# Kernel optimization log

Hardware: AMD Instinct MI355X
Metric: run time of the kernel (lower is better)

Reference implementation:

```python
import jax, jax.numpy as jnp
import numpy as np

MC = 16384
N_STEPS = 120
PERIOD = 30
N_MAT = 4
N_STR = 21
WIDTH_DIFF = 50
WIDTH_VAN = 30
WIDTH_EXO = 20
N_HIDDEN = 3  # n_layers=4 -> input layer + 3 hidden layers + output layer
R = 0.05
TIMEGRID = jnp.asarray(np.linspace(0.0, 1.0, N_STEPS + 1).astype(np.float32))
STRIKES = jnp.asarray(np.linspace(0.8, 1.2, N_STR).astype(np.float32))


def _init_net(key, d_in, width, d_out):
    ks = jax.random.split(key, 6)
    f = lambda k, shape, fan: jax.random.normal(k, shape, jnp.float32) / np.sqrt(fan).astype(np.float32)
    return dict(
        W0=f(ks[0], (N_MAT, d_in, width), d_in),
        b0=f(ks[1], (N_MAT, width), width),
        hW=f(ks[2], (N_MAT, N_HIDDEN, width, width), width),
        hb=f(ks[3], (N_MAT, N_HIDDEN, width), width),
        Wo=f(ks[4], (N_MAT, width, d_out), width),
        bo=f(ks[5], (N_MAT, d_out), width),
    )


def setup_inputs() -> dict:
    key = jax.random.key(0)
    kz, kd, kv, ke = jax.random.split(key, 4)
    inp = {
        "S0": jnp.ones((1,), jnp.float32),
        "z": jax.random.normal(kz, (MC, N_STEPS), jnp.float32),
    }
    for name, net in (("d", _init_net(kd, 2, WIDTH_DIFF, 1)),
                      ("v", _init_net(kv, 2, WIDTH_VAN, N_STR * N_MAT)),
                      ("e", _init_net(ke, N_STEPS + 2, WIDTH_EXO, 1))):
        for pn, arr in net.items():
            inp[name + pn] = arr
    inp["MC_samples"] = MC
    inp["ind_T"] = N_STEPS
    inp["period_length"] = PERIOD
    return inp


def _mlp(x, W0, b0, hW, hb, Wo, bo, softplus_out):
    h = jax.nn.relu(x @ W0 + b0)
    for k in range(hW.shape[0]):  # static small number of hidden layers
        h = jax.nn.relu(h @ hW[k] + hb[k])
    y = h @ Wo + bo
    return jax.nn.softplus(y) if softplus_out else y


def _forward(S0, z, dW0, db0, dhW, dhb, dWo, dbo,
             vW0, vb0, vhW, vhb, vWo, vbo,
             eW0, eb0, ehW, ehb, eWo, ebo,
             MC_samples, ind_T, period_length, remat=False):
    sg = jax.lax.stop_gradient
    S_init = jnp.ones((MC_samples, 1), jnp.float32) * S0
    path0 = jnp.zeros((MC_samples, N_STEPS + 1), jnp.float32).at[:, 0].set(S_init[:, 0])
    zeros_mat = jnp.zeros((N_MAT, N_STR), jnp.float32)

    def step(carry, i):
        S_old, cv_v, cv_e, run_max, path, pv, pvv = carry
        idx = (i - 1) // period_length
        t0 = TIMEGRID[i - 1]
        h = TIMEGRID[i] - TIMEGRID[i - 1]
        sqh = jnp.sqrt(h)
        dWn = sqh * jax.lax.dynamic_slice_in_dim(z, i - 1, 1, 1)  # (MC,1)
        t = jnp.full_like(S_old, t0)
        diff = _mlp(jnp.concatenate([t, S_old], 1),
                    dW0[idx], db0[idx], dhW[idx], dhb[idx], dWo[idx], dbo[idx], True)
        Sd, diffd = sg(S_old), sg(diff)
        S_new = (S_old
                 + R * S_old * h / (1.0 + R * Sd * sqh)
                 + S_old * diff * dWn / (1.0 + Sd * diffd * sqh))
        disc = jnp.exp(-R * t0)
        cv_v = cv_v + disc * Sd * diffd * dWn * _mlp(
            jnp.concatenate([t, Sd], 1),
            vW0[idx], vb0[idx], vhW[idx], vhb[idx], vWo[idx], vbo[idx], False)
        cv_e = cv_e + disc * Sd * diffd * dWn * _mlp(
            jnp.concatenate([t, path], 1),
            eW0[idx], eb0[idx], ehW[idx], ehb[idx], eWo[idx], ebo[idx], False)
        path = jax.lax.dynamic_update_slice(path, sg(S_new), (0, i))
        run_max = jnp.maximum(run_max, S_new)
        # vanilla prices at maturities (i multiple of period_length)
        ind_m = i // period_length - 1
        disc_i = jnp.exp(-R * TIMEGRID[i])
        cv_row = jax.lax.dynamic_slice_in_dim(
            cv_v.reshape(MC_samples, N_MAT, N_STR), ind_m, 1, 1)[:, 0, :]
        pr = disc_i * jnp.maximum(S_new - STRIKES[None, :], 0.0) - cv_row  # (MC, N_STR)
        is_mat = (i % period_length) == 0
        pv = jnp.where(is_mat, jax.lax.dynamic_update_index_in_dim(pv, pr.mean(0), ind_m, 0), pv)
        pvv = jnp.where(is_mat, jax.lax.dynamic_update_index_in_dim(pvv, jnp.var(pr, axis=0, ddof=1), ind_m, 0), pvv)
        return (S_new, cv_v, cv_e, run_max, path, pv, pvv), None

    body = jax.checkpoint(step) if remat else step
    carry0 = (S_init,
              jnp.zeros((MC_samples, N_STR * N_MAT), jnp.float32),
              jnp.zeros((MC_samples, 1), jnp.float32),
              S_init, path0, zeros_mat, zeros_mat)
    (S_T, cv_v, cv_e, run_max, path, pv, pvv), _ = jax.lax.scan(
        body, carry0, jnp.arange(1, ind_T + 1))

    sgv = jax.lax.stop_gradient
    exotic = run_max - S_T
    discT = jnp.exp(-R * TIMEGRID[ind_T])
    e = discT * exotic
    error = sgv(e) - jnp.mean(sgv(e)) - sgv(cv_e)
    price_exo = e - cv_e
    return pv, pvv, price_exo, price_exo.mean(), jnp.var(price_exo, ddof=1), error


def reference(S0, z, dW0, db0, dhW, dhb, dWo, dbo,
              vW0, vb0, vhW, vhb, vWo, vbo,
              eW0, eb0, ehW, ehb, eWo, ebo,
              MC_samples, ind_T, period_length):
    return _forward(S0, z, dW0, db0, dhW, dhb, dWo, dbo,
                    vW0, vb0, vhW, vhb, vWo, vbo,
                    eW0, eb0, ehW, ehb, eWo, ebo,
                    MC_samples, ind_T, period_length)
```

## Files before the change

### kernel.cpp

```cpp
#include <hip/hip_runtime.h>
#include <hip/hip_bf16.h>
#include <math.h>

#define MC      16384
#define NSTEPS  120
#define PER     30
#define NMAT    4
#define NSTR    21
#define RRATE   0.05f
#define NBLK    512
#define NSAMP   32
#define HSTEP   (1.0f/120.0f)
#define SQH     0.09128709291752769f

typedef short short8  __attribute__((ext_vector_type(8)));
typedef short short4v __attribute__((ext_vector_type(4)));
typedef float f32x4   __attribute__((ext_vector_type(4)));

#define WS_PRPART 0
#define WS_EPART  (NMAT*NSTR*2*NBLK)
#define WS_MEANE  (WS_EPART + NBLK)

#define OUT_PV    0
#define OUT_PVV   84
#define OUT_PEXO  168
#define OUT_MEAN  16552
#define OUT_VAR   16553
#define OUT_ERR   16554

__device__ __forceinline__ float tgridf(int i)  { return (float)i * HSTEP; }
__device__ __forceinline__ float strikef(int s) { return (float)(0.8 + (double)s * 0.02); }
__device__ __forceinline__ float softplusf(float x){
  return fmaxf(x, 0.0f) + __logf(1.0f + __expf(-fabsf(x)));
}
__device__ __forceinline__ unsigned short f2bf(float f){
  __hip_bfloat16 b = __float2bfloat16(f);
  return __builtin_bit_cast(unsigned short, b);
}
__device__ __forceinline__ float bf2f(unsigned short u){
  return __builtin_bit_cast(float, ((unsigned)u)<<16);
}
__device__ __forceinline__ int swaddr(int row, int slot, int inner){
  return row*256 + (((slot + row) & 15) << 4) + inner;
}
__device__ __forceinline__ short8 rdA(const unsigned short* H, int mt, int base, int lane){
  int addr = swaddr(mt*16 + (lane&15), base + (lane>>4), 0);
  return *(const short8*)((const char*)H + addr);
}
__device__ __forceinline__ f32x4 mm(short8 a, short8 b, f32x4 c){
  return __builtin_amdgcn_mfma_f32_16x16x32_bf16(a, b, c, 0, 0, 0);
}
__device__ __forceinline__ void stD(unsigned short* H, int colbase, int mt, int lane,
                                    f32x4 acc, bool relu){
  int col  = colbase + (lane & 15);
  int slot = col >> 3, inner = (col & 7)*2;
  #pragma unroll
  for (int i2=0;i2<4;++i2){
    int rw = mt*16 + ((lane>>4)<<2) + i2;
    float v = acc[i2];
    if (relu) v = fmaxf(v, 0.0f);
    *(unsigned short*)((char*)H + swaddr(rw, slot, inner)) = f2bf(v);
  }
}
__device__ __forceinline__ short8 mkBd(const float* __restrict__ W, const float* __restrict__ bias,
                                       int n0, int kt, int lane){
  short8 r;
  int n = n0 + (lane&15);
  #pragma unroll
  for (int i2=0;i2<8;++i2){
    int k = kt*32 + ((lane>>4)<<3) + i2;
    float w;
    if (k<50)       w = (n<50)? W[k*50+n] : 0.f;
    else if (k==50) w = (n<50)? bias[n] : ((n==50)? 1.f : 0.f);
    else            w = 0.f;
    r[i2] = (short)f2bf(w);
  }
  return r;
}
__device__ __forceinline__ short8 mkBq(const float* __restrict__ W, const float* __restrict__ bias,
                                       int KV, int n0, int lane){
  short8 r;
  int n = n0 + (lane&15);
  #pragma unroll
  for (int i2=0;i2<8;++i2){
    int k = ((lane>>4)<<3) + i2;
    float w;
    if (k<KV)       w = (n<KV)? W[k*KV+n] : 0.f;
    else if (k==KV) w = (n<KV)? bias[n] : ((n==KV)? 1.f : 0.f);
    else            w = 0.f;
    r[i2] = (short)f2bf(w);
  }
  return r;
}

extern "C" __global__ void __launch_bounds__(256,2) mc_main(
    const float* __restrict__ S0p, const float* __restrict__ z,
    const float* __restrict__ dW0, const float* __restrict__ db0,
    const float* __restrict__ dhW, const float* __restrict__ dhb,
    const float* __restrict__ dWo, const float* __restrict__ dbo,
    const float* __restrict__ vW0, const float* __restrict__ vb0,
    const float* __restrict__ vhW, const float* __restrict__ vhb,
    const float* __restrict__ vWo, const float* __restrict__ vbo,
    const float* __restrict__ eW0, const float* __restrict__ eb0,
    const float* __restrict__ ehW, const float* __restrict__ ehb,
    const float* __restrict__ eWo, const float* __restrict__ ebo,
    float* __restrict__ out, float* __restrict__ ws)
{
  __shared__ unsigned short Hb0[NSAMP*128];
  __shared__ unsigned short Hb1[NSAMP*128];
  __shared__ short8 BqL[4][3][64];
  __shared__ short8 BdL[4][6][64];
  __shared__ float vh3f[NSAMP*40];
  __shared__ float zper[NSAMP*30];
  __shared__ float eW0per[NMAT*600];
  __shared__ float dW0s[128];
  __shared__ float db0s[64];
  __shared__ float vW0s[64];
  __shared__ float vb0s[32];
  __shared__ float eW0ts[20];
  __shared__ float eb0s[20];
  __shared__ float dWoL[64];
  __shared__ float eWoL[32];
  __shared__ float dtab[PER];
  __shared__ float Sb[NSAMP], ebuf[NSAMP];
  __shared__ float part[2*84*2];

  const int tid  = threadIdx.x;
  const int lane = tid & 63;
  const int wid  = __builtin_amdgcn_readfirstlane(tid >> 6);
  const int blk  = blockIdx.x;
  const int r    = tid >> 3;
  const int cc   = tid & 7;

  const int  ntd = wid;
  const bool isv = (wid < 2);
  const int  ntq = wid & 1;

  const float S0v = S0p[0];
  float S = S0v, runmax = S0v, cvE = 0.f;
  f32x4 rr[3];
  #pragma unroll
  for (int q=0;q<3;++q){ rr[q][0]=0.f; rr[q][1]=0.f; rr[q][2]=0.f; rr[q][3]=0.f; }
  float aE[NMAT][4];
  #pragma unroll
  for (int mt2=0;mt2<NMAT;++mt2){ aE[mt2][0]=0.f; aE[mt2][1]=0.f; aE[mt2][2]=0.f; aE[mt2][3]=0.f; }
  float G_[4] = {0.f,0.f,0.f,0.f};

  #pragma unroll 1
  for (int p=0;p<NMAT;++p){
    for (int q=tid; q<NSAMP*30; q+=256){ int r2=q/30, c2=q%30; zper[q] = z[(size_t)(blk*NSAMP+r2)*NSTEPS + p*30 + c2]; }
    for (int q=tid; q<NMAT*600; q+=256){ int mat=q/600, k=q%600; eW0per[q] = eW0[mat*2440 + p*600 + 20 + k]; }
    if (tid < 128){
      int rw = tid>>6, j = tid&63;
      dW0s[tid] = (j<50)? dW0[p*100 + rw*50 + j] : 0.f;
    } else if (tid < 192){
      int j = tid-128;
      db0s[j] = (j<50)? db0[p*50+j] : ((j==50)? 1.f : 0.f);
    } else {
      int idx = tid-192, rw = idx>>5, j = idx&31;
      vW0s[idx] = (j<30)? vW0[p*60 + rw*30 + j] : 0.f;
    }
    if (tid < 32)       vb0s[tid] = (tid<30)? vb0[p*30+tid] : ((tid==30)? 1.f : 0.f);
    else if (tid < 52){ int j=tid-32; eW0ts[j]=eW0[p*2440+j]; eb0s[j]=eb0[p*20+j]; }
    else if (tid < 116){ int j=tid-52; dWoL[j] = (j<50)? dWo[p*50+j] : 0.f; }
    else if (tid < 148){ int j=tid-116; eWoL[j] = (j<20)? eWo[p*20+j] : 0.f; }
    else if (tid < 148+PER){ int j=tid-148; dtab[j] = __expf(-RRATE * ((float)(p*PER+j) * HSTEP)); }

    const float dboS = dbo[p], eboS = ebo[p];

    const float* dhWp = dhW + p*7500;
    const float* dhbp = dhb + p*150;
    BdL[wid][0][lane] = mkBd(dhWp,      dhbp,     ntd*16, 0, lane);
    BdL[wid][1][lane] = mkBd(dhWp,      dhbp,     ntd*16, 1, lane);
    BdL[wid][2][lane] = mkBd(dhWp+2500, dhbp+50,  ntd*16, 0, lane);
    BdL[wid][3][lane] = mkBd(dhWp+2500, dhbp+50,  ntd*16, 1, lane);
    BdL[wid][4][lane] = mkBd(dhWp+5000, dhbp+100, ntd*16, 0, lane);
    BdL[wid][5][lane] = mkBd(dhWp+5000, dhbp+100, ntd*16, 1, lane);
    {
      const float* qW    = isv ? (vhW + p*2700) : (ehW + p*1200);
      const float* qb    = isv ? (vhb + p*90)   : (ehb + p*60);
      const int    qstep = isv ? 900 : 400;
      const int    qN    = isv ? 30  : 20;
      BqL[wid][0][lane] = mkBq(qW,         qb,        qN, ntq*16, lane);
      BqL[wid][1][lane] = mkBq(qW+qstep,   qb+qN,     qN, ntq*16, lane);
      BqL[wid][2][lane] = mkBq(qW+2*qstep, qb+2*qN,   qN, ntq*16, lane);
    }
    const int qbase = isv ? 8 : 12;
    const int qcolb = (isv?64:96) + ntq*16;

    __syncthreads();

    #pragma unroll 1
    for (int ii=1; ii<=PER; ++ii){
      const float t0  = tgridf(p*PER + ii - 1);

      {
        short8 hv;
        #pragma unroll
        for (int k=0;k<8;++k){
          int j = cc*8 + k;
          float u = fmaxf(fmaf(t0, dW0s[j], fmaf(S, dW0s[64+j], db0s[j])), 0.f);
          hv[k] = (short)f2bf(u);
        }
        *(short8*)((char*)Hb0 + swaddr(r, cc, 0)) = hv;
        short4v vv;
        #pragma unroll
        for (int k=0;k<4;++k){
          int j = cc*4 + k;
          float u = fmaxf(fmaf(t0, vW0s[j], fmaf(S, vW0s[32+j], vb0s[j])), 0.f);
          vv[k] = (short)f2bf(u);
        }
        *(short4v*)((char*)Hb0 + swaddr(r, 8+(cc>>1), (cc&1)*8)) = vv;
        short4v ev = {0,0,0,0};
        if (cc < 5){
          const int o = (ii-1)*20 + cc*4;
          f32x4 w0 = *(const f32x4*)&eW0per[        o];
          f32x4 w1 = *(const f32x4*)&eW0per[ 600 +  o];
          f32x4 w2 = *(const f32x4*)&eW0per[1200 +  o];
          f32x4 w3 = *(const f32x4*)&eW0per[1800 +  o];
          #pragma unroll
          for (int k=0;k<4;++k){
            aE[0][k] = fmaf(S, w0[k], aE[0][k]);
            aE[1][k] = fmaf(S, w1[k], aE[1][k]);
            aE[2][k] = fmaf(S, w2[k], aE[2][k]);
            aE[3][k] = fmaf(S, w3[k], aE[3][k]);
            float a = (p==0)?aE[0][k]:(p==1)?aE[1][k]:(p==2)?aE[2][k]:aE[3][k];
            int j = cc*4 + k;
            float e0 = fmaxf(t0*eW0ts[j] + a + eb0s[j], 0.f);
            ev[k] = (short)f2bf(e0);
          }
        } else if (cc == 5){
          ev[0] = (short)0x3F80;
        }
        *(short4v*)((char*)Hb0 + swaddr(r, 12+(cc>>1), (cc&1)*8)) = ev;
      }
      __syncthreads();
      {
        short8 b0 = BdL[wid][0][lane], b1 = BdL[wid][1][lane];
        short8 a00=rdA(Hb0,0,0,lane), a01=rdA(Hb0,0,4,lane);
        short8 a10=rdA(Hb0,1,0,lane), a11=rdA(Hb0,1,4,lane);
        f32x4 c0={0.f,0.f,0.f,0.f}, c1={0.f,0.f,0.f,0.f};
        c0=mm(a00,b0,c0); c0=mm(a01,b1,c0);
        c1=mm(a10,b0,c1); c1=mm(a11,b1,c1);
        stD(Hb1, ntd*16, 0, lane, c0, true);
        stD(Hb1, ntd*16, 1, lane, c1, true);
        short8 Bq = BqL[wid][0][lane];
        short8 q0=rdA(Hb0,0,qbase,lane), q1=rdA(Hb0,1,qbase,lane);
        f32x4 cq0={0.f,0.f,0.f,0.f}, cq1={0.f,0.f,0.f,0.f};
        cq0=mm(q0,Bq,cq0); cq1=mm(q1,Bq,cq1);
        stD(Hb1, qcolb, 0, lane, cq0, true);
        stD(Hb1, qcolb, 1, lane, cq1, true);
      }
      __syncthreads();
      {
        short8 b0 = BdL[wid][2][lane], b1 = BdL[wid][3][lane];
        short8 a00=rdA(Hb1,0,0,lane), a01=rdA(Hb1,0,4,lane);
        short8 a10=rdA(Hb1,1,0,lane), a11=rdA(Hb1,1,4,lane);
        f32x4 c0={0.f,0.f,0.f,0.f}, c1={0.f,0.f,0.f,0.f};
        c0=mm(a00,b0,c0); c0=mm(a01,b1,c0);
        c1=mm(a10,b0,c1); c1=mm(a11,b1,c1);
        stD(Hb0, ntd*16, 0, lane, c0, true);
        stD(Hb0, ntd*16, 1, lane, c1, true);
        short8 Bq = BqL[wid][1][lane];
        short8 q0=rdA(Hb1,0,qbase,lane), q1=rdA(Hb1,1,qbase,lane);
        f32x4 cq0={0.f,0.f,0.f,0.f}, cq1={0.f,0.f,0.f,0.f};
        cq0=mm(q0,Bq,cq0); cq1=mm(q1,Bq,cq1);
        stD(Hb0, qcolb, 0, lane, cq0, true);
        stD(Hb0, qcolb, 1, lane, cq1, true);
      }
      __syncthreads();
      {
        short8 b0 = BdL[wid][4][lane], b1 = BdL[wid][5][lane];
        short8 a00=rdA(Hb0,0,0,lane), a01=rdA(Hb0,0,4,lane);
        short8 a10=rdA(Hb0,1,0,lane), a11=rdA(Hb0,1,4,lane);
        f32x4 c0={0.f,0.f,0.f,0.f}, c1={0.f,0.f,0.f,0.f};
        c0=mm(a00,b0,c0); c0=mm(a01,b1,c0);
        c1=mm(a10,b0,c1); c1=mm(a11,b1,c1);
        stD(Hb1, ntd*16, 0, lane, c0, true);
        stD(Hb1, ntd*16, 1, lane, c1, true);
        short8 Bq = BqL[wid][2][lane];
        short8 q0=rdA(Hb0,0,qbase,lane), q1=rdA(Hb0,1,qbase,lane);
        f32x4 cq0={0.f,0.f,0.f,0.f}, cq1={0.f,0.f,0.f,0.f};
        cq0=mm(q0,Bq,cq0); cq1=mm(q1,Bq,cq1);
        if (isv){
          #pragma unroll
          for (int i2=0;i2<4;++i2){
            int r0 = ((lane>>4)<<2) + i2;
            vh3f[ r0     *40 + ntq*16 + (lane&15)] = fmaxf(cq0[i2], 0.f);
            vh3f[(16+r0) *40 + ntq*16 + (lane&15)] = fmaxf(cq1[i2], 0.f);
          }
        } else {
          stD(Hb1, qcolb, 0, lane, cq0, true);
          stD(Hb1, qcolb, 1, lane, cq1, true);
        }
      }
      __syncthreads();
      {
        float yp = 0.f;
        {
          short8 hv = *(const short8*)((const char*)Hb1 + swaddr(r, cc, 0));
          #pragma unroll
          for (int k=0;k<8;++k) yp = fmaf(bf2f((unsigned short)hv[k]), dWoL[cc*8+k], yp);
        }
        float yep = 0.f;
        if (cc < 5){
          short4v hv = *(const short4v*)((const char*)Hb1 + swaddr(r, 12+(cc>>1), (cc&1)*8));
          #pragma unroll
          for (int k=0;k<4;++k) yep = fmaf(bf2f((unsigned short)hv[k]), eWoL[cc*4+k], yep);
        }
        #pragma unroll
        for (int mk=1; mk<8; mk<<=1){ yp += __shfl_xor(yp, mk); yep += __shfl_xor(yep, mk); }
        const float y    = yp + dboS;
        const float diff = softplusf(y);
        const float zv   = zper[r*30 + (ii-1)];
        const float dWn  = SQH * zv;
        const float d1 = 1.f + (RRATE*SQH)*S;
        const float d2 = 1.f + S*diff*SQH;
        const float Snew = S + (RRATE*HSTEP)*S*__builtin_amdgcn_rcpf(d1)
                             + S*diff*dWn*__builtin_amdgcn_rcpf(d2);
        const float disc = dtab[ii-1];
        const float coef = disc * S * diff * dWn;
        cvE = fmaf(coef, yep + eboS, cvE);
        runmax = fmaxf(runmax, Snew);
        {
          f32x4 vv = *(const f32x4*)&vh3f[r*40 + cc*4];
          #pragma unroll
          for (int k=0;k<4;++k) G_[k] = fmaf(coef, vv[k], G_[k]);
        }
        S = Snew;

        if (ii==PER){
          short4v gv;
          #pragma unroll
          for (int k=0;k<4;++k){ gv[k] = (short)f2bf(G_[k]); G_[k] = 0.f; }
          *(short4v*)((char*)Hb0 + swaddr(r, cc>>1, (cc&1)*8)) = gv;
          if (cc==0) Sb[r] = S;
        }
      }

      if (ii==PER){
        __syncthreads();
        const float disc_i = __expf(-RRATE * ((float)(p+1) * 0.25f));
        const float* vWop = vWo + p*2520;
        const float* vbop = vbo + p*84;
        #pragma unroll
        for (int q3=0;q3<3;++q3){
          const int T = wid*3 + q3;
          const int mtr = T/6, ntr = T%6;
          short8 a = rdA(Hb0, mtr, 0, lane);
          const int col = ntr*16 + (lane&15);
          short8 bw;
          #pragma unroll
          for (int i2=0;i2<8;++i2){
            int k = ((lane>>4)<<3)+i2;
            float w = 0.f;
            if (col < 84){
              if (k < 30)       w = vWop[k*84+col];
              else if (k == 30) w = vbop[col];
            }
            bw[i2] = (short)f2bf(w);
          }
          f32x4 d4 = {0.f,0.f,0.f,0.f};
          d4 = mm(a,bw,d4);
          const int s = col - p*NSTR;
          const bool inr = (s>=0) && (s<NSTR) && (col<84);
          const float K = strikef(s);
          float ssum=0.f, ssq=0.f;
          #pragma unroll
          for (int i2=0;i2<4;++i2){
            int row = mtr*16 + ((lane>>4)<<2) + i2;
            rr[q3][i2] += d4[i2];
            if (inr){
              float pr = disc_i*fmaxf(Sb[row]-K,0.f) - rr[q3][i2];
              ssum += pr; ssq = fmaf(pr,pr,ssq);
            }
          }
          ssum += __shfl_down(ssum,16); ssum += __shfl_down(ssum,32);
          ssq  += __shfl_down(ssq ,16); ssq  += __shfl_down(ssq ,32);
          if (inr && lane<16){
            part[(mtr*84+col)*2+0] = ssum;
            part[(mtr*84+col)*2+1] = ssq;
          }
        }
        __syncthreads();
        if (tid < NSTR){
          int cidx = p*NSTR + tid;
          ws[WS_PRPART + (cidx*2+0)*NBLK + blk] = part[cidx*2] + part[(84+cidx)*2];
        } else if (tid >= 64 && tid < 64+NSTR){
          int cidx = p*NSTR + (tid-64);
          ws[WS_PRPART + (cidx*2+1)*NBLK + blk] = part[cidx*2+1] + part[(84+cidx)*2+1];
        }
        __syncthreads();
      }
    }
  }

  if (cc==0){
    const float discT = __expf(-RRATE);
    const float e = discT * (runmax - S);
    out[OUT_PEXO + blk*NSAMP + r] = e - cvE;
    ebuf[r] = e;
  }
  __syncthreads();
  if (tid < 32){
    float se = ebuf[tid];
    se += __shfl_down(se,16); se += __shfl_down(se,8);
    se += __shfl_down(se,4);  se += __shfl_down(se,2); se += __shfl_down(se,1);
    if (tid==0) ws[WS_EPART + blk] = se;
  }
}

extern "C" __global__ void fin_pv(const float* __restrict__ ws, float* __restrict__ out){
  const int t = threadIdx.x;
  if (t >= NMAT*NSTR) return;
  float sum=0.0f, ssq=0.0f;
  for (int b=0;b<NBLK;++b){
    sum += ws[WS_PRPART + (t*2+0)*NBLK + b];
    ssq += ws[WS_PRPART + (t*2+1)*NBLK + b];
  }
  out[OUT_PV  + t] = sum * (1.0f/MC);
  out[OUT_PVV + t] = (ssq - sum*sum*(1.0f/MC)) * (1.0f/(MC-1));
}

extern "C" __global__ void fin_pe(float* out, float* ws){
  __shared__ float sA[4], sB[4], sC[4];
  const int t = threadIdx.x;
  float sum=0.0f, ssq=0.0f;
  for (int idx=t; idx<MC; idx+=256){
    const float v = out[OUT_PEXO+idx];
    sum += v; ssq = fmaf(v,v,ssq);
  }
  float es = ws[WS_EPART + t] + ws[WS_EPART + 256 + t];
  for (int o=32;o>0;o>>=1){
    sum += __shfl_down(sum,o);
    ssq += __shfl_down(ssq,o);
    es  += __shfl_down(es,o);
  }
  const int w=t>>6, lane=t&63;
  if (lane==0){ sA[w]=sum; sB[w]=ssq; sC[w]=es; }
  __syncthreads();
  if (t==0){
    const float s=sA[0]+sA[1]+sA[2]+sA[3];
    const float q=sB[0]+sB[1]+sB[2]+sB[3];
    const float e=sC[0]+sC[1]+sC[2]+sC[3];
    out[OUT_MEAN]=s*(1.0f/MC);
    out[OUT_VAR]=(q - s*s*(1.0f/MC))*(1.0f/(MC-1));
    ws[WS_MEANE]=e*(1.0f/MC);
  }
}

extern "C" __global__ void fin_err(float* out, const float* __restrict__ ws){
  const int m = blockIdx.x*blockDim.x + threadIdx.x;
  if (m < MC) out[OUT_ERR+m] = out[OUT_PEXO+m] - ws[WS_MEANE];
}

extern "C" void kernel_launch(void* const* d_in, const int* in_sizes, int n_in,
                              void* d_out, int out_size, void* d_ws, size_t ws_size,
                              hipStream_t stream){
  (void)in_sizes; (void)n_in; (void)out_size; (void)ws_size;
  const float* S0 =(const float*)d_in[0];
  const float* z  =(const float*)d_in[1];
  const float* dW0=(const float*)d_in[2];
  const float* db0=(const float*)d_in[3];
  const float* dhW=(const float*)d_in[4];
  const float* dhb=(const float*)d_in[5];
  const float* dWo=(const float*)d_in[6];
  const float* dbo=(const float*)d_in[7];
  const float* vW0=(const float*)d_in[8];
  const float* vb0=(const float*)d_in[9];
  const float* vhW=(const float*)d_in[10];
  const float* vhb=(const float*)d_in[11];
  const float* vWo=(const float*)d_in[12];
  const float* vbo=(const float*)d_in[13];
  const float* eW0=(const float*)d_in[14];
  const float* eb0=(const float*)d_in[15];
  const float* ehW=(const float*)d_in[16];
  const float* ehb=(const float*)d_in[17];
  const float* eWo=(const float*)d_in[18];
  const float* ebo=(const float*)d_in[19];
  float* out=(float*)d_out;
  float* ws =(float*)d_ws;

  mc_main<<<dim3(NBLK),dim3(256),0,stream>>>(S0,z,dW0,db0,dhW,dhb,dWo,dbo,
                                             vW0,vb0,vhW,vhb,vWo,vbo,
                                             eW0,eb0,ehW,ehb,eWo,ebo,out,ws);
  fin_pv <<<dim3(1), dim3(128),0,stream>>>(ws,out);
  fin_pe <<<dim3(1), dim3(256),0,stream>>>(out,ws);
  fin_err<<<dim3(64),dim3(256),0,stream>>>(out,ws);
}
```

Baseline: 445.3 us.

## Precompute MFMA weight fragments in a separate kernel and load from global

Adds a small pre-kernel that builds the bf16 MFMA B-fragments for all hidden layers of the three networks once and writes them to the workspace. The main kernel drops its per-block shared-memory fragment arrays and instead reloads the fragments from global memory (L2/L1 resident) at every timestep, with launch bounds raised from 2 to 3 blocks per CU. This removes redundant fragment construction in each block and frees LDS to allow higher occupancy, at the cost of repeated global loads inside the inner loop and one extra kernel launch.

```diff
diff --git a/kernel.cpp b/kernel.cpp
--- a/kernel.cpp
+++ b/kernel.cpp
@@ -20,6 +20,7 @@
 #define WS_PRPART 0
 #define WS_EPART  (NMAT*NSTR*2*NBLK)
 #define WS_MEANE  (WS_EPART + NBLK)
+#define WS_FRAGS  86784
 
 #define OUT_PV    0
 #define OUT_PVV   84
@@ -93,7 +94,31 @@
   return r;
 }
 
-extern "C" __global__ void __launch_bounds__(256,2) mc_main(
+extern "C" __global__ void mk_frags(
+    const float* __restrict__ dhW, const float* __restrict__ dhb,
+    const float* __restrict__ vhW, const float* __restrict__ vhb,
+    const float* __restrict__ ehW, const float* __restrict__ ehb,
+    float* __restrict__ ws)
+{
+  const int bid = blockIdx.x;
+  const int p   = bid / 36;
+  const int fid = bid % 36;
+  const int lane = threadIdx.x;
+  short8 fr;
+  if (fid < 24){
+    int l = fid >> 3, nt = (fid >> 1) & 3, kt = fid & 1;
+    fr = mkBd(dhW + p*7500 + l*2500, dhb + p*150 + l*50, nt*16, kt, lane);
+  } else if (fid < 30){
+    int q = fid - 24, l = q >> 1, nt = q & 1;
+    fr = mkBq(vhW + p*2700 + l*900, vhb + p*90 + l*30, 30, nt*16, lane);
+  } else {
+    int q = fid - 30, l = q >> 1, nt = q & 1;
+    fr = mkBq(ehW + p*1200 + l*400, ehb + p*60 + l*20, 20, nt*16, lane);
+  }
+  ((short8*)(ws + WS_FRAGS))[(p*36 + fid)*64 + lane] = fr;
+}
+
+extern "C" __global__ void __launch_bounds__(256,3) mc_main(
     const float* __restrict__ S0p, const float* __restrict__ z,
     const float* __restrict__ dW0, const float* __restrict__ db0,
     const float* __restrict__ dhW, const float* __restrict__ dhb,
@@ -108,8 +133,6 @@
 {
   __shared__ unsigned short Hb0[NSAMP*128];
   __shared__ unsigned short Hb1[NSAMP*128];
-  __shared__ short8 BqL[4][3][64];
-  __shared__ short8 BdL[4][6][64];
   __shared__ float vh3f[NSAMP*40];
   __shared__ float zper[NSAMP*30];
   __shared__ float eW0per[NMAT*600];
@@ -132,8 +155,8 @@
   const int r    = tid >> 3;
   const int cc   = tid & 7;
 
+  const bool isv = (wid < 2);
   const int  ntd = wid;
-  const bool isv = (wid < 2);
   const int  ntq = wid & 1;
 
   const float S0v = S0p[0];
@@ -167,32 +190,17 @@
     else if (tid < 148+PER){ int j=tid-148; dtab[j] = __expf(-RRATE * ((float)(p*PER+j) * HSTEP)); }
 
     const float dboS = dbo[p], eboS = ebo[p];
-
-    const float* dhWp = dhW + p*7500;
-    const float* dhbp = dhb + p*150;
-    BdL[wid][0][lane] = mkBd(dhWp,      dhbp,     ntd*16, 0, lane);
-    BdL[wid][1][lane] = mkBd(dhWp,      dhbp,     ntd*16, 1, lane);
-    BdL[wid][2][lane] = mkBd(dhWp+2500, dhbp+50,  ntd*16, 0, lane);
-    BdL[wid][3][lane] = mkBd(dhWp+2500, dhbp+50,  ntd*16, 1, lane);
-    BdL[wid][4][lane] = mkBd(dhWp+5000, dhbp+100, ntd*16, 0, lane);
-    BdL[wid][5][lane] = mkBd(dhWp+5000, dhbp+100, ntd*16, 1, lane);
-    {
-      const float* qW    = isv ? (vhW + p*2700) : (ehW + p*1200);
-      const float* qb    = isv ? (vhb + p*90)   : (ehb + p*60);
-      const int    qstep = isv ? 900 : 400;
-      const int    qN    = isv ? 30  : 20;
-      BqL[wid][0][lane] = mkBq(qW,         qb,        qN, ntq*16, lane);
-      BqL[wid][1][lane] = mkBq(qW+qstep,   qb+qN,     qN, ntq*16, lane);
-      BqL[wid][2][lane] = mkBq(qW+2*qstep, qb+2*qN,   qN, ntq*16, lane);
-    }
-    const int qbase = isv ? 8 : 12;
-    const int qcolb = (isv?64:96) + ntq*16;
+    const int fqB = (isv? 24 : 30) + ntq;
 
     __syncthreads();
 
     #pragma unroll 1
     for (int ii=1; ii<=PER; ++ii){
       const float t0  = tgridf(p*PER + ii - 1);
+
+      const short8* FB;
+      { uintptr_t u = (uintptr_t)(ws + WS_FRAGS); asm volatile("" : "+s"(u)); FB = (const short8*)u; }
+      const short8* FBp = FB + (size_t)p*36*64 + lane;
 
       {
         short8 hv;
@@ -236,7 +244,8 @@
       }
       __syncthreads();
       {
-        short8 b0 = BdL[wid][0][lane], b1 = BdL[wid][1][lane];
+        short8 b0 = FBp[(0 + ntd*2 + 0)*64], b1 = FBp[(0 + ntd*2 + 1)*64];
+        short8 Bq = FBp[fqB*64];
         short8 a00=rdA(Hb0,0,0,lane), a01=rdA(Hb0,0,4,lane);
         short8 a10=rdA(Hb0,1,0,lane), a11=rdA(Hb0,1,4,lane);
         f32x4 c0={0.f,0.f,0.f,0.f}, c1={0.f,0.f,0.f,0.f};
@@ -244,16 +253,16 @@
         c1=mm(a10,b0,c1); c1=mm(a11,b1,c1);
         stD(Hb1, ntd*16, 0, lane, c0, true);
         stD(Hb1, ntd*16, 1, lane, c1, true);
-        short8 Bq = BqL[wid][0][lane];
-        short8 q0=rdA(Hb0,0,qbase,lane), q1=rdA(Hb0,1,qbase,lane);
+        short8 q0=rdA(Hb0,0,isv?8:12,lane), q1=rdA(Hb0,1,isv?8:12,lane);
         f32x4 cq0={0.f,0.f,0.f,0.f}, cq1={0.f,0.f,0.f,0.f};
         cq0=mm(q0,Bq,cq0); cq1=mm(q1,Bq,cq1);
-        stD(Hb1, qcolb, 0, lane, cq0, true);
-        stD(Hb1, qcolb, 1, lane, cq1, true);
+        stD(Hb1, (isv?64:96)+ntq*16, 0, lane, cq0, true);
+        stD(Hb1, (isv?64:96)+ntq*16, 1, lane, cq1, true);
       }
       __syncthreads();
       {
-        short8 b0 = BdL[wid][2][lane], b1 = BdL[wid][3][lane];
+        short8 b0 = FBp[(8 + ntd*2 + 0)*64], b1 = FBp[(8 + ntd*2 + 1)*64];
+        short8 Bq = FBp[(fqB+2)*64];
         short8 a00=rdA(Hb1,0,0,lane), a01=rdA(Hb1,0,4,lane);
         short8 a10=rdA(Hb1,1,0,lane), a11=rdA(Hb1,1,4,lane);
         f32x4 c0={0.f,0.f,0.f,0.f}, c1={0.f,0.f,0.f,0.f};
@@ -261,16 +270,16 @@
         c1=mm(a10,b0,c1); c1=mm(a11,b1,c1);
         stD(Hb0, ntd*16, 0, lane, c0, true);
         stD(Hb0, ntd*16, 1, lane, c1, true);
-        short8 Bq = BqL[wid][1][lane];
-        short8 q0=rdA(Hb1,0,qbase,lane), q1=rdA(Hb1,1,qbase,lane);
+        short8 q0=rdA(Hb1,0,isv?8:12,lane), q1=rdA(Hb1,1,isv?8:12,lane);
         f32x4 cq0={0.f,0.f,0.f,0.f}, cq1={0.f,0.f,0.f,0.f};
         cq0=mm(q0,Bq,cq0); cq1=mm(q1,Bq,cq1);
-        stD(Hb0, qcolb, 0, lane, cq0, true);
-        stD(Hb0, qcolb, 1, lane, cq1, true);
+        stD(Hb0, (isv?64:96)+ntq*16, 0, lane, cq0, true);
+        stD(Hb0, (isv?64:96)+ntq*16, 1, lane, cq1, true);
       }
       __syncthreads();
       {
-        short8 b0 = BdL[wid][4][lane], b1 = BdL[wid][5][lane];
+        short8 b0 = FBp[(16 + ntd*2 + 0)*64], b1 = FBp[(16 + ntd*2 + 1)*64];
+        short8 Bq = FBp[(fqB+4)*64];
         short8 a00=rdA(Hb0,0,0,lane), a01=rdA(Hb0,0,4,lane);
         short8 a10=rdA(Hb0,1,0,lane), a11=rdA(Hb0,1,4,lane);
         f32x4 c0={0.f,0.f,0.f,0.f}, c1={0.f,0.f,0.f,0.f};
@@ -278,8 +287,7 @@
         c1=mm(a10,b0,c1); c1=mm(a11,b1,c1);
         stD(Hb1, ntd*16, 0, lane, c0, true);
         stD(Hb1, ntd*16, 1, lane, c1, true);
-        short8 Bq = BqL[wid][2][lane];
-        short8 q0=rdA(Hb0,0,qbase,lane), q1=rdA(Hb0,1,qbase,lane);
+        short8 q0=rdA(Hb0,0,isv?8:12,lane), q1=rdA(Hb0,1,isv?8:12,lane);
         f32x4 cq0={0.f,0.f,0.f,0.f}, cq1={0.f,0.f,0.f,0.f};
         cq0=mm(q0,Bq,cq0); cq1=mm(q1,Bq,cq1);
         if (isv){
@@ -290,8 +298,8 @@
             vh3f[(16+r0) *40 + ntq*16 + (lane&15)] = fmaxf(cq1[i2], 0.f);
           }
         } else {
-          stD(Hb1, qcolb, 0, lane, cq0, true);
-          stD(Hb1, qcolb, 1, lane, cq1, true);
+          stD(Hb1, 96+ntq*16, 0, lane, cq0, true);
+          stD(Hb1, 96+ntq*16, 1, lane, cq1, true);
         }
       }
       __syncthreads();
@@ -481,6 +489,7 @@
   float* out=(float*)d_out;
   float* ws =(float*)d_ws;
 
+  mk_frags<<<dim3(NMAT*36),dim3(64),0,stream>>>(dhW,dhb,vhW,vhb,ehW,ehb,ws);
   mc_main<<<dim3(NBLK),dim3(256),0,stream>>>(S0,z,dW0,db0,dhW,dhb,dWo,dbo,
                                              vW0,vb0,vhW,vhb,vWo,vbo,
                                              eW0,eb0,ehW,ehb,eWo,ebo,out,ws);
```

Measured after the change: 492.3 us. 10.6% more time.
